# Kernel optimization log

Hardware: AMD Instinct MI355X
Metric: run time of the kernel (lower is better)

## Reference

```python
import jax, jax.numpy as jnp
import numpy as np
import math

D_MODEL = 2048
N_HEADS = 16
HEAD_DIM = D_MODEL // N_HEADS  # 128
SEQ_LEN = 4096
BATCH = 4


def rotate_half(x):
    x1, x2 = x[..., : x.shape[-1] // 2], x[..., x.shape[-1] // 2 :]
    return jnp.concatenate((-x2, x1), axis=-1)


def rope_cos_sin(seq_len, head_dim, dtype=jnp.float32):
    inv_freq = 1.0 / (10000.0 ** (jnp.arange(0, head_dim, 2, dtype=jnp.float32) / head_dim))
    freqs = jnp.arange(seq_len, dtype=jnp.float32)[:, None] * inv_freq[None, :]  # [S, D/2]
    emb = jnp.concatenate((freqs, freqs), axis=-1)  # [S, D]
    return jnp.cos(emb).astype(dtype), jnp.sin(emb).astype(dtype)


def setup_inputs() -> dict:
    key = jax.random.key(0)
    kx, kq, kk, kv = jax.random.split(key, 4)
    x = jax.random.normal(kx, (BATCH, SEQ_LEN, D_MODEL), dtype=jnp.float32)
    s = 1.0 / math.sqrt(D_MODEL)
    # torch Linear weight: [out_features, in_features]
    w_q = jax.random.uniform(kq, (HEAD_DIM, D_MODEL), minval=-s, maxval=s, dtype=jnp.float32)
    w_k = jax.random.uniform(kk, (HEAD_DIM, D_MODEL), minval=-s, maxval=s, dtype=jnp.float32)
    w_v = jax.random.uniform(kv, (HEAD_DIM, D_MODEL), minval=-s, maxval=s, dtype=jnp.float32)
    return {"x": x, "w_q": w_q, "w_k": w_k, "w_v": w_v}


def reference(x, w_q, w_k, w_v):
    B, S, _ = x.shape
    scale = 1.0 / math.sqrt(HEAD_DIM)
    # projections: x @ W^T  -> [B, S, head_dim]
    q = jnp.einsum('bsd,hd->bsh', x, w_q)
    k = jnp.einsum('bsd,hd->bsh', x, w_k)
    v = jnp.einsum('bsd,hd->bsh', x, w_v)
    cos, sin = rope_cos_sin(S, HEAD_DIM, x.dtype)  # [S, head_dim]
    q = q * cos + rotate_half(q) * sin
    k = k * cos + rotate_half(k) * sin
    scores = jnp.einsum('bqh,bkh->bqk', q, k) * scale  # [B, S, S]
    causal = jnp.tril(jnp.ones((S, S), dtype=bool))
    scores = jnp.where(causal[None, :, :], scores, -jnp.inf)
    attn = jax.nn.softmax(scores, axis=-1)
    out = jnp.einsum('bqk,bkh->bqh', attn, v)  # [B, S, head_dim]
    return out
```

## Files before the change

### kernel.cpp

```cpp
#include <hip/hip_runtime.h>
#include <hip/hip_bf16.h>

#define BATCH 4
#define SEQ 4096
#define DMODEL 2048
#define HD 128
#define BS (BATCH*SEQ)

typedef __attribute__((ext_vector_type(8))) short short8;
typedef __attribute__((ext_vector_type(4))) short short4v;
typedef __attribute__((ext_vector_type(4))) float f32x4;
typedef __attribute__((ext_vector_type(4))) float float4v;
typedef unsigned short u16;
typedef unsigned int u32;

#define LOG2E 1.4426950408889634f
#define SCALE 0.08838834764831845f

__device__ __forceinline__ u16 f2bf(float f){
  u32 u = __builtin_bit_cast(u32, f);
  u32 r = (u + 0x7FFFu + ((u >> 16) & 1u)) >> 16;
  return (u16)r;
}

__device__ __forceinline__ void gload16(const void* gptr, void* lptr){
  __builtin_amdgcn_global_load_lds((const __attribute__((address_space(1))) void*)gptr,
                                   (__attribute__((address_space(3))) void*)lptr, 16, 0, 0);
}

__global__ __launch_bounds__(256) void k_tab(float2* __restrict__ tab){
  int i = blockIdx.x*256 + threadIdx.x;
  int s = i >> 6, j = i & 63;
  float invf = (float)pow(10000.0, -(double)j/64.0);
  float ang  = (float)s * invf;
  double a = (double)ang;
  tab[i] = make_float2((float)cos(a), (float)sin(a));
}

__global__ __launch_bounds__(256) void k_cvtw(const float* __restrict__ wq, const float* __restrict__ wk,
                                              const float* __restrict__ wv, u16* __restrict__ wb){
  int i = blockIdx.x*256 + threadIdx.x;
  int m = i >> 18; int r = i & 262143;
  const float* s = (m==0) ? wq : ((m==1) ? wk : wv);
  wb[i] = f2bf(s[r]);
}

__global__ __launch_bounds__(256,2) void k_gemm(
    const float* __restrict__ x, const u16* __restrict__ wb, const float2* __restrict__ tab,
    u16* __restrict__ qb, u16* __restrict__ kb, u16* __restrict__ vt)
{
  __shared__ char lds[32768];
  const int tid = threadIdx.x;
  const int bid = blockIdx.x;
  const int xcd = bid & 7, idx = bid >> 3;
  const int mloc = idx / 3, ng = idx - mloc*3;
  const int mg = xcd*16 + mloc;
  const size_t M0 = (size_t)mg * 128;
  const u16* Wm = wb + (size_t)ng * (HD*DMODEL);
  const int w = tid >> 6, lane = tid & 63, lr = lane & 15, lg = lane >> 4;

  const float* aptr[8];
  int awb[8];
  #pragma unroll
  for (int i=0;i<8;i++){
    int L = i*4096 + tid*16;
    int row = L >> 8, col = (L & 255) >> 2;
    aptr[i] = x + (M0 + row)*DMODEL + col;
    awb[i]  = row*128 + ((col*2) ^ ((row & 7) << 4));
  }
  int woff[4], wdst[4];
  #pragma unroll
  for (int i=0;i<4;i++){
    int L = i*4096 + tid*16;
    int row = L >> 7, cb = L & 127;
    int scb = cb ^ ((row & 7) << 4);
    woff[i] = row*DMODEL + (scb >> 1);
    wdst[i] = 16384 + L;
  }

  f32x4 acc[2][8];
  #pragma unroll
  for (int i=0;i<2;i++)
    #pragma unroll
    for (int j=0;j<8;j++) acc[i][j] = f32x4{0.f,0.f,0.f,0.f};

  for (int t=0; t<32; t++){
    const int k0 = t*64;
    float4v av[8];
    #pragma unroll
    for (int i=0;i<8;i++) av[i] = *(const float4v*)(aptr[i] + k0);
    #pragma unroll
    for (int i=0;i<4;i++) gload16(Wm + woff[i] + k0, lds + wdst[i]);
    #pragma unroll
    for (int i=0;i<8;i++){
      short4v o;
      o[0]=(short)f2bf(av[i][0]); o[1]=(short)f2bf(av[i][1]);
      o[2]=(short)f2bf(av[i][2]); o[3]=(short)f2bf(av[i][3]);
      *(short4v*)(lds + awb[i]) = o;
    }
    __syncthreads();
    short8 afr[2][2], bfr[8][2];
    #pragma unroll
    for (int rf=0; rf<2; rf++)
      #pragma unroll
      for (int ks=0; ks<2; ks++){
        int r = w*32 + rf*16 + lr;
        afr[rf][ks] = *(const short8*)(lds + r*128 + ((ks*64 + lg*16) ^ ((r&7)<<4)));
      }
    #pragma unroll
    for (int nf=0; nf<8; nf++)
      #pragma unroll
      for (int ks=0; ks<2; ks++){
        int r = nf*16 + lr;
        bfr[nf][ks] = *(const short8*)(lds + 16384 + r*128 + ((ks*64 + lg*16) ^ ((r&7)<<4)));
      }
    #pragma unroll
    for (int rf=0; rf<2; rf++)
      #pragma unroll
      for (int nf=0; nf<8; nf++){
        acc[rf][nf] = __builtin_amdgcn_mfma_f32_16x16x32_bf16(afr[rf][0], bfr[nf][0], acc[rf][nf], 0,0,0);
        acc[rf][nf] = __builtin_amdgcn_mfma_f32_16x16x32_bf16(afr[rf][1], bfr[nf][1], acc[rf][nf], 0,0,0);
      }
    __syncthreads();
  }

  if (ng < 2){
    u16* dst = (ng == 0) ? qb : kb;
    #pragma unroll
    for (int rf=0; rf<2; rf++){
      #pragma unroll
      for (int reg=0; reg<4; reg++){
        size_t grow = M0 + w*32 + rf*16 + lg*4 + reg;
        int spos = (int)(grow & (SEQ-1));
        #pragma unroll
        for (int cf=0; cf<4; cf++){
          int j = cf*16 + lr;
          float2 cs = tab[spos*64 + j];
          float lo = acc[rf][cf][reg];
          float hi = acc[rf][cf+4][reg];
          dst[grow*HD + j]      = f2bf(lo*cs.x - hi*cs.y);
          dst[grow*HD + j + 64] = f2bf(hi*cs.x + lo*cs.y);
        }
      }
    }
  } else {
    #pragma unroll
    for (int rf=0; rf<2; rf++)
      #pragma unroll
      for (int reg=0; reg<4; reg++){
        size_t grow = M0 + w*32 + rf*16 + lg*4 + reg;
        size_t b = grow >> 12;
        size_t spos = grow & (SEQ-1);
        #pragma unroll
        for (int cf=0; cf<8; cf++){
          int col = cf*16 + lr;
          vt[(b*HD + col)*SEQ + spos] = f2bf(acc[rf][cf][reg]);
        }
      }
  }
}

__global__ __launch_bounds__(256) void k_attn(
    const u16* __restrict__ qbuf, const u16* __restrict__ kb, const u16* __restrict__ vt,
    float* __restrict__ Opart, float2* __restrict__ ml)
{
  __shared__ u16 lK[64*128];
  __shared__ u16 lV[128*64];
  __shared__ u16 lP[4][16*64];
  const int tid = threadIdx.x;
  const int bid = blockIdx.x;
  const int x = bid & 7, idx = bid >> 3;
  const int b = x >> 1, half = x & 1;
  const int qt = 63 - (idx >> 1);
  const int sp = (idx & 1) + 2*half;
  const int qbn = b*64 + qt;
  const int w = tid >> 6, lane = tid & 63, lr = lane & 15, lg = lane >> 4;

  const int n = qt + 1, cbase = n >> 2, crem = n & 3;
  const int cnt = cbase + (sp < crem ? 1 : 0);
  const int klo = sp*cbase + (sp < crem ? sp : crem);
  const int khi = klo + cnt;
  const size_t prow0 = ((size_t)qbn*4 + sp)*64;

  if (cnt == 0){
    if (lr == 0){
      #pragma unroll
      for (int reg=0; reg<4; reg++)
        ml[prow0 + w*16 + lg*4 + reg] = make_float2(-1e30f, 0.f);
    }
    return;
  }

  const size_t qrow = (size_t)b*SEQ + qt*64 + w*16 + lr;
  short8 aq[4];
  #pragma unroll
  for (int ks=0; ks<4; ks++)
    aq[ks] = *(const short8*)(qbuf + qrow*HD + ks*32 + lg*8);

  f32x4 accO[8];
  #pragma unroll
  for (int i=0;i<8;i++) accO[i] = f32x4{0.f,0.f,0.f,0.f};
  float m2[4]   = {-1e30f,-1e30f,-1e30f,-1e30f};
  float lsum[4] = {0.f,0.f,0.f,0.f};

  const int Lb = tid*16;
  const float cfac = SCALE * LOG2E;

  for (int kt = klo; kt < khi; kt++){
    #pragma unroll
    for (int i=0;i<4;i++){
      int L = i*4096 + Lb;
      { int row = L >> 8, cb = L & 255;
        int scb = cb ^ ((row & 7) << 4);
        gload16(kb + ((size_t)b*SEQ + kt*64 + row)*HD + (scb>>1), ((char*)lK) + L); }
      { int row = L >> 7, cb = L & 127;
        int scb = cb ^ ((row & 7) << 4);
        gload16(vt + ((size_t)b*HD + row)*SEQ + kt*64 + (scb>>1), ((char*)lV) + L); }
    }
    __syncthreads();

    f32x4 sc[4];
    #pragma unroll
    for (int nf=0; nf<4; nf++){
      sc[nf] = f32x4{0.f,0.f,0.f,0.f};
      #pragma unroll
      for (int ks=0; ks<4; ks++){
        int r = nf*16 + lr;
        int byte = r*256 + ((ks*64 + lg*16) ^ ((r&7)<<4));
        short8 bk = *(const short8*)((const char*)lK + byte);
        sc[nf] = __builtin_amdgcn_mfma_f32_16x16x32_bf16(aq[ks], bk, sc[nf], 0,0,0);
      }
      sc[nf] *= cfac;
    }
    if (kt == qt){
      #pragma unroll
      for (int nf=0; nf<4; nf++)
        #pragma unroll
        for (int reg=0; reg<4; reg++){
          int col = nf*16 + lr;
          int row = w*16 + lg*4 + reg;
          if (col > row) sc[nf][reg] = -1e30f;
        }
    }
    float al[4];
    #pragma unroll
    for (int reg=0; reg<4; reg++){
      float v = fmaxf(fmaxf(sc[0][reg], sc[1][reg]), fmaxf(sc[2][reg], sc[3][reg]));
      v = fmaxf(v, __shfl_xor(v, 1));
      v = fmaxf(v, __shfl_xor(v, 2));
      v = fmaxf(v, __shfl_xor(v, 4));
      v = fmaxf(v, __shfl_xor(v, 8));
      float mnew = fmaxf(m2[reg], v);
      al[reg] = exp2f(m2[reg] - mnew);
      m2[reg] = mnew;
    }
    float prs[4] = {0.f,0.f,0.f,0.f};
    #pragma unroll
    for (int nf=0; nf<4; nf++)
      #pragma unroll
      for (int reg=0; reg<4; reg++){
        float p = exp2f(sc[nf][reg] - m2[reg]);
        prs[reg] += p;
        int r = lg*4 + reg;
        int byte = r*128 + ((nf*32 + lr*2) ^ ((r&7)<<4));
        *(u16*)(((char*)lP[w]) + byte) = f2bf(p);
      }
    f32x4 alv = f32x4{al[0], al[1], al[2], al[3]};
    #pragma unroll
    for (int reg=0; reg<4; reg++){
      float v = prs[reg];
      v += __shfl_xor(v, 1);
      v += __shfl_xor(v, 2);
      v += __shfl_xor(v, 4);
      v += __shfl_xor(v, 8);
      lsum[reg] = lsum[reg]*al[reg] + v;
    }
    #pragma unroll
    for (int cf=0; cf<8; cf++) accO[cf] *= alv;

    short8 pa[2];
    #pragma unroll
    for (int ks=0; ks<2; ks++){
      int byte = lr*128 + ((ks*64 + lg*16) ^ ((lr&7)<<4));
      pa[ks] = *(const short8*)(((const char*)lP[w]) + byte);
    }
    #pragma unroll
    for (int cf=0; cf<8; cf++){
      #pragma unroll
      for (int ks=0; ks<2; ks++){
        int d = cf*16 + lr;
        int byte = d*128 + ((ks*64 + lg*16) ^ ((d&7)<<4));
        short8 bv = *(const short8*)(((const char*)lV) + byte);
        accO[cf] = __builtin_amdgcn_mfma_f32_16x16x32_bf16(pa[ks], bv, accO[cf], 0,0,0);
      }
    }
    __syncthreads();
  }

  #pragma unroll
  for (int reg=0; reg<4; reg++){
    size_t pr = prow0 + w*16 + lg*4 + reg;
    #pragma unroll
    for (int cf=0; cf<8; cf++)
      Opart[pr*HD + cf*16 + lr] = accO[cf][reg];
  }
  if (lr == 0){
    #pragma unroll
    for (int reg=0; reg<4; reg++)
      ml[prow0 + w*16 + lg*4 + reg] = make_float2(m2[reg], lsum[reg]);
  }
}

__global__ __launch_bounds__(256) void k_comb(
    const float* __restrict__ Opart, const float2* __restrict__ ml, float* __restrict__ out)
{
  const int t = threadIdx.x;
  const int r = blockIdx.x*8 + (t >> 5);
  const int c = (t & 31)*4;
  const int qbn = r >> 6, rr = r & 63;
  float m[4], l[4], M = -1e30f;
  #pragma unroll
  for (int s=0; s<4; s++){
    float2 v = ml[((size_t)qbn*4 + s)*64 + rr];
    m[s] = v.x; l[s] = v.y;
    M = fmaxf(M, m[s]);
  }
  float L = 0.f;
  #pragma unroll
  for (int s=0; s<4; s++){ m[s] = exp2f(m[s] - M); L += l[s]*m[s]; }
  const float inv = 1.0f / L;
  f32x4 acc = f32x4{0.f,0.f,0.f,0.f};
  #pragma unroll
  for (int s=0; s<4; s++){
    f32x4 o = *(const f32x4*)(Opart + (((size_t)qbn*4 + s)*64 + rr)*(size_t)HD + c);
    float sc = m[s]*inv;
    acc += o * sc;
  }
  *(f32x4*)(out + (size_t)r*HD + c) = acc;
}

extern "C" void kernel_launch(void* const* d_in, const int* in_sizes, int n_in,
                              void* d_out, int out_size, void* d_ws, size_t ws_size,
                              hipStream_t stream){
  const float* x  = (const float*)d_in[0];
  const float* wq = (const float*)d_in[1];
  const float* wk = (const float*)d_in[2];
  const float* wv = (const float*)d_in[3];
  float* out = (float*)d_out;
  char* ws = (char*)d_ws;

  size_t off = 0;
  u16* wb = (u16*)(ws + off); off += (size_t)3*HD*DMODEL*2;
  float2* tab = (float2*)(ws + off); off += (size_t)SEQ*64*8;
  u16* qb = (u16*)(ws + off); off += (size_t)BS*HD*2;
  u16* kb = (u16*)(ws + off); off += (size_t)BS*HD*2;
  u16* vt = (u16*)(ws + off); off += (size_t)BS*HD*2;
  float* Opart = (float*)(ws + off); off += (size_t)1024*64*HD*4;
  float2* ml   = (float2*)(ws + off); off += (size_t)1024*64*8;
  if (ws_size < off) return;

  hipLaunchKernelGGL(k_tab,  dim3(1024),  dim3(256), 0, stream, tab);
  hipLaunchKernelGGL(k_cvtw, dim3(3072),  dim3(256), 0, stream, wq, wk, wv, wb);
  hipLaunchKernelGGL(k_gemm, dim3(384),   dim3(256), 0, stream, x, wb, tab, qb, kb, vt);
  hipLaunchKernelGGL(k_attn, dim3(1024),  dim3(256), 0, stream, qb, kb, vt, Opart, ml);
  hipLaunchKernelGGL(k_comb, dim3(2048),  dim3(256), 0, stream, Opart, ml, out);
}
```

Baseline: 122.4 us.

## Double-buffer projection GEMM and split N into 64-wide tiles for more blocks

The QKV projection GEMM now uses double-buffered LDS, prefetching the next K-slice of x and W while MFMAs run on the current one, so only one barrier per iteration remains. The N dimension is split into 64-column tiles, giving 768 blocks instead of 384, and occupancy rises to 3 blocks per CU. To let a 64-wide tile apply RoPE locally, the weight conversion kernel permutes Q/K rows so each tile holds matching lo/hi rotate-half pairs. The cost is that x is read twice as often and the LDS footprint is larger.

```diff
diff --git a/kernel.cpp b/kernel.cpp
--- a/kernel.cpp
+++ b/kernel.cpp
@@ -8,7 +8,6 @@
 #define BS (BATCH*SEQ)
 
 typedef __attribute__((ext_vector_type(8))) short short8;
-typedef __attribute__((ext_vector_type(4))) short short4v;
 typedef __attribute__((ext_vector_type(4))) float f32x4;
 typedef __attribute__((ext_vector_type(4))) float float4v;
 typedef unsigned short u16;
@@ -40,109 +39,141 @@
 __global__ __launch_bounds__(256) void k_cvtw(const float* __restrict__ wq, const float* __restrict__ wk,
                                               const float* __restrict__ wv, u16* __restrict__ wb){
   int i = blockIdx.x*256 + threadIdx.x;
-  int m = i >> 18; int r = i & 262143;
-  const float* s = (m==0) ? wq : ((m==1) ? wk : wv);
-  wb[i] = f2bf(s[r]);
-}
-
-__global__ __launch_bounds__(256,2) void k_gemm(
+  int r = i >> 11, k = i & 2047;
+  const float* s; int sr;
+  if (r < 256){
+    s = (r < 128) ? wq : wk;
+    int rr = r & 127, blk = rr >> 6, c = rr & 63;
+    sr = blk*32 + (c & 31) + ((c >> 5) << 6);
+  } else {
+    s = wv; sr = r - 256;
+  }
+  wb[i] = f2bf(s[sr*2048 + k]);
+}
+
+__global__ __launch_bounds__(256,3) void k_gemm(
     const float* __restrict__ x, const u16* __restrict__ wb, const float2* __restrict__ tab,
     u16* __restrict__ qb, u16* __restrict__ kb, u16* __restrict__ vt)
 {
-  __shared__ char lds[32768];
+  __shared__ char lds[49152];
   const int tid = threadIdx.x;
   const int bid = blockIdx.x;
   const int xcd = bid & 7, idx = bid >> 3;
-  const int mloc = idx / 3, ng = idx - mloc*3;
+  const int mloc = idx / 6, ng = idx - mloc*6;
   const int mg = xcd*16 + mloc;
   const size_t M0 = (size_t)mg * 128;
-  const u16* Wm = wb + (size_t)ng * (HD*DMODEL);
   const int w = tid >> 6, lane = tid & 63, lr = lane & 15, lg = lane >> 4;
 
-  const float* aptr[8];
-  int awb[8];
-  #pragma unroll
-  for (int i=0;i<8;i++){
+  const float* aptr[4];
+  int awb[4];
+  #pragma unroll
+  for (int i=0;i<4;i++){
     int L = i*4096 + tid*16;
-    int row = L >> 8, col = (L & 255) >> 2;
-    aptr[i] = x + (M0 + row)*DMODEL + col;
-    awb[i]  = row*128 + ((col*2) ^ ((row & 7) << 4));
-  }
-  int woff[4], wdst[4];
-  #pragma unroll
-  for (int i=0;i<4;i++){
+    int row = L >> 7, colb = L & 127;
+    aptr[i] = x + (M0 + row)*DMODEL + (colb >> 1);
+    awb[i]  = row*128 + (colb ^ ((row & 7) << 4));
+  }
+  int woff[2], wdst[2];
+  #pragma unroll
+  for (int i=0;i<2;i++){
     int L = i*4096 + tid*16;
     int row = L >> 7, cb = L & 127;
     int scb = cb ^ ((row & 7) << 4);
-    woff[i] = row*DMODEL + (scb >> 1);
-    wdst[i] = 16384 + L;
-  }
-
-  f32x4 acc[2][8];
+    woff[i] = (ng*64 + row)*DMODEL + (scb >> 1);
+    wdst[i] = 32768 + L;
+  }
+
+  f32x4 acc[2][4];
   #pragma unroll
   for (int i=0;i<2;i++)
     #pragma unroll
-    for (int j=0;j<8;j++) acc[i][j] = f32x4{0.f,0.f,0.f,0.f};
+    for (int j=0;j<4;j++) acc[i][j] = f32x4{0.f,0.f,0.f,0.f};
+
+  #pragma unroll
+  for (int i=0;i<2;i++) gload16(wb + woff[i], lds + wdst[i]);
+  #pragma unroll
+  for (int i=0;i<4;i++){
+    float4v a0 = *(const float4v*)(aptr[i]);
+    float4v a1 = *(const float4v*)(aptr[i] + 4);
+    short8 o;
+    o[0]=(short)f2bf(a0[0]); o[1]=(short)f2bf(a0[1]); o[2]=(short)f2bf(a0[2]); o[3]=(short)f2bf(a0[3]);
+    o[4]=(short)f2bf(a1[0]); o[5]=(short)f2bf(a1[1]); o[6]=(short)f2bf(a1[2]); o[7]=(short)f2bf(a1[3]);
+    *(short8*)(lds + awb[i]) = o;
+  }
+  __syncthreads();
 
   for (int t=0; t<32; t++){
-    const int k0 = t*64;
+    const int p = t & 1;
     float4v av[8];
-    #pragma unroll
-    for (int i=0;i<8;i++) av[i] = *(const float4v*)(aptr[i] + k0);
-    #pragma unroll
-    for (int i=0;i<4;i++) gload16(Wm + woff[i] + k0, lds + wdst[i]);
-    #pragma unroll
-    for (int i=0;i<8;i++){
-      short4v o;
-      o[0]=(short)f2bf(av[i][0]); o[1]=(short)f2bf(av[i][1]);
-      o[2]=(short)f2bf(av[i][2]); o[3]=(short)f2bf(av[i][3]);
-      *(short4v*)(lds + awb[i]) = o;
+    if (t < 31){
+      const int k0 = (t+1)*64;
+      #pragma unroll
+      for (int i=0;i<4;i++){
+        av[2*i]   = *(const float4v*)(aptr[i] + k0);
+        av[2*i+1] = *(const float4v*)(aptr[i] + k0 + 4);
+      }
+      #pragma unroll
+      for (int i=0;i<2;i++) gload16(wb + woff[i] + k0, lds + wdst[i] + (p^1)*8192);
+    }
+    {
+      const char* lA = lds + p*16384;
+      const char* lW = lds + 32768 + p*8192;
+      short8 af[2][2], wf[4][2];
+      #pragma unroll
+      for (int rf=0; rf<2; rf++)
+        #pragma unroll
+        for (int ks=0; ks<2; ks++){
+          int r = w*32 + rf*16 + lr;
+          af[rf][ks] = *(const short8*)(lA + r*128 + ((ks*64 + lg*16) ^ ((r&7)<<4)));
+        }
+      #pragma unroll
+      for (int nf=0; nf<4; nf++)
+        #pragma unroll
+        for (int ks=0; ks<2; ks++){
+          int r = nf*16 + lr;
+          wf[nf][ks] = *(const short8*)(lW + r*128 + ((ks*64 + lg*16) ^ ((r&7)<<4)));
+        }
+      #pragma unroll
+      for (int rf=0; rf<2; rf++)
+        #pragma unroll
+        for (int nf=0; nf<4; nf++){
+          acc[rf][nf] = __builtin_amdgcn_mfma_f32_16x16x32_bf16(af[rf][0], wf[nf][0], acc[rf][nf], 0,0,0);
+          acc[rf][nf] = __builtin_amdgcn_mfma_f32_16x16x32_bf16(af[rf][1], wf[nf][1], acc[rf][nf], 0,0,0);
+        }
+    }
+    if (t < 31){
+      #pragma unroll
+      for (int i=0;i<4;i++){
+        short8 o;
+        o[0]=(short)f2bf(av[2*i][0]);   o[1]=(short)f2bf(av[2*i][1]);
+        o[2]=(short)f2bf(av[2*i][2]);   o[3]=(short)f2bf(av[2*i][3]);
+        o[4]=(short)f2bf(av[2*i+1][0]); o[5]=(short)f2bf(av[2*i+1][1]);
+        o[6]=(short)f2bf(av[2*i+1][2]); o[7]=(short)f2bf(av[2*i+1][3]);
+        *(short8*)(lds + (p^1)*16384 + awb[i]) = o;
+      }
     }
     __syncthreads();
-    short8 afr[2][2], bfr[8][2];
+  }
+
+  if (ng < 4){
+    u16* dst = (ng >> 1) ? kb : qb;
+    const int half = ng & 1;
     #pragma unroll
     for (int rf=0; rf<2; rf++)
-      #pragma unroll
-      for (int ks=0; ks<2; ks++){
-        int r = w*32 + rf*16 + lr;
-        afr[rf][ks] = *(const short8*)(lds + r*128 + ((ks*64 + lg*16) ^ ((r&7)<<4)));
-      }
-    #pragma unroll
-    for (int nf=0; nf<8; nf++)
-      #pragma unroll
-      for (int ks=0; ks<2; ks++){
-        int r = nf*16 + lr;
-        bfr[nf][ks] = *(const short8*)(lds + 16384 + r*128 + ((ks*64 + lg*16) ^ ((r&7)<<4)));
-      }
-    #pragma unroll
-    for (int rf=0; rf<2; rf++)
-      #pragma unroll
-      for (int nf=0; nf<8; nf++){
-        acc[rf][nf] = __builtin_amdgcn_mfma_f32_16x16x32_bf16(afr[rf][0], bfr[nf][0], acc[rf][nf], 0,0,0);
-        acc[rf][nf] = __builtin_amdgcn_mfma_f32_16x16x32_bf16(afr[rf][1], bfr[nf][1], acc[rf][nf], 0,0,0);
-      }
-    __syncthreads();
-  }
-
-  if (ng < 2){
-    u16* dst = (ng == 0) ? qb : kb;
-    #pragma unroll
-    for (int rf=0; rf<2; rf++){
       #pragma unroll
       for (int reg=0; reg<4; reg++){
         size_t grow = M0 + w*32 + rf*16 + lg*4 + reg;
         int spos = (int)(grow & (SEQ-1));
         #pragma unroll
-        for (int cf=0; cf<4; cf++){
-          int j = cf*16 + lr;
+        for (int nf=0; nf<2; nf++){
+          int j = half*32 + nf*16 + lr;
           float2 cs = tab[spos*64 + j];
-          float lo = acc[rf][cf][reg];
-          float hi = acc[rf][cf+4][reg];
+          float lo = acc[rf][nf][reg];
+          float hi = acc[rf][nf+2][reg];
           dst[grow*HD + j]      = f2bf(lo*cs.x - hi*cs.y);
           dst[grow*HD + j + 64] = f2bf(hi*cs.x + lo*cs.y);
         }
       }
-    }
   } else {
     #pragma unroll
     for (int rf=0; rf<2; rf++)
@@ -152,9 +183,9 @@
         size_t b = grow >> 12;
         size_t spos = grow & (SEQ-1);
         #pragma unroll
-        for (int cf=0; cf<8; cf++){
-          int col = cf*16 + lr;
-          vt[(b*HD + col)*SEQ + spos] = f2bf(acc[rf][cf][reg]);
+        for (int nf=0; nf<4; nf++){
+          int vcol = (ng-4)*64 + nf*16 + lr;
+          vt[(b*HD + vcol)*SEQ + spos] = f2bf(acc[rf][nf][reg]);
         }
       }
   }
@@ -361,7 +392,7 @@
 
   hipLaunchKernelGGL(k_tab,  dim3(1024),  dim3(256), 0, stream, tab);
   hipLaunchKernelGGL(k_cvtw, dim3(3072),  dim3(256), 0, stream, wq, wk, wv, wb);
-  hipLaunchKernelGGL(k_gemm, dim3(384),   dim3(256), 0, stream, x, wb, tab, qb, kb, vt);
+  hipLaunchKernelGGL(k_gemm, dim3(768),   dim3(256), 0, stream, x, wb, tab, qb, kb, vt);
   hipLaunchKernelGGL(k_attn, dim3(1024),  dim3(256), 0, stream, qb, kb, vt, Opart, ml);
   hipLaunchKernelGGL(k_comb, dim3(2048),  dim3(256), 0, stream, Opart, ml, out);
 }
```

Result: no change. 123.3 us (+0.8%).
